# Kernel optimization log

Measured on AMD Instinct MI355X. Metric: run time of the kernel, lower is better.

## Reference

```python
import jax, jax.numpy as jnp
import numpy as np

B, DIM, H, W = 2, 256, 64, 64
HEADS, DIM_HEAD = 8, 64
DIM_INNER = HEADS * DIM_HEAD  # 512


def setup_inputs() -> dict:
    key = jax.random.key(0)
    k1, k2, k3 = jax.random.split(key, 3)
    fmap = jax.random.normal(k1, (B, DIM, H, W), dtype=jnp.float32)
    # 1x1 convs == channel matmuls; store as [out_ch, in_ch]
    w_qkv = jax.random.normal(k2, (3 * DIM_INNER, DIM), dtype=jnp.float32) * (DIM ** -0.5)
    w_out = jax.random.normal(k3, (DIM, DIM_INNER), dtype=jnp.float32) * (DIM_INNER ** -0.5)
    return {"fmap": fmap, "w_qkv": w_qkv, "w_out": w_out}


def reference(fmap, w_qkv, w_out):
    b, c, x, y = fmap.shape
    n = x * y
    h, d = HEADS, DIM_HEAD
    xt = fmap.reshape(b, c, n)                       # [B, C, N]
    qkv = jnp.einsum('oc,bcn->bon', w_qkv, xt)        # [B, 3*h*d, N]
    q, k, v = jnp.split(qkv, 3, axis=1)               # each [B, h*d, N]
    # -> [B, h, N, d]
    to_bhnd = lambda t: t.reshape(b, h, d, n).transpose(0, 1, 3, 2)
    q, k, v = to_bhnd(q), to_bhnd(k), to_bhnd(v)
    # Euclidean distance matrix (torch.cdist p=2)
    q2 = jnp.sum(q * q, axis=-1)                      # [B, h, N]
    k2 = jnp.sum(k * k, axis=-1)                      # [B, h, N]
    qk = jnp.einsum('bhid,bhjd->bhij', q, k)          # [B, h, N, N]
    sim = jnp.sqrt(jnp.maximum(q2[..., :, None] + k2[..., None, :] - 2.0 * qk, 0.0))
    attn = jax.nn.softmax(sim, axis=-1)
    out = jnp.einsum('bhij,bhjd->bhid', attn, v)      # [B, h, N, d]
    out = out.transpose(0, 1, 3, 2).reshape(b, h * d, n)  # [B, h*d, N]
    out = jnp.einsum('oc,bcn->bon', w_out, out)       # [B, dim, N]
    return out.reshape(b, c, x, y)
```

## Files before the change

kernel.cpp:

```cpp
#include <hip/hip_runtime.h>

#define B_      2
#define DIM_    256
#define N_      4096
#define HEADS_  8
#define DINNER_ 512

typedef _Float16 half_t;
typedef _Float16 half8  __attribute__((ext_vector_type(8)));
typedef _Float16 half4v __attribute__((ext_vector_type(4)));
typedef _Float16 half2v __attribute__((ext_vector_type(2)));
typedef float    floatx4 __attribute__((ext_vector_type(4)));

#define SCL_    1.4426950408889634f
#define SHIFT2_ 20.0f


__global__ __launch_bounds__(256) void prep_all(const float* __restrict__ fmap,
                                                const float* __restrict__ w_qkv,
                                                const float* __restrict__ w_out,
                                                half_t* __restrict__ wqF,
                                                half_t* __restrict__ woF,
                                                half_t* __restrict__ xTg) {
    const int t = threadIdx.x, bx = blockIdx.x;
    __shared__ float Tl[64 * 68];
    if (bx < 96) {
        half_t* dst = wqF + (size_t)bx * 4096;
#pragma unroll
        for (int j = 0; j < 2; ++j) {
            const int cch = j * 256 + t;
            const int o = cch >> 4, m15 = cch & 15;
            const float4 a  = *(const float4*)&w_qkv[(size_t)(bx * 16 + m15) * 256 + o * 8];
            const float4 bb = *(const float4*)&w_qkv[(size_t)(bx * 16 + m15) * 256 + o * 8 + 4];
            half8 hv;
            hv[0] = (half_t)a.x;  hv[1] = (half_t)a.y;  hv[2] = (half_t)a.z;  hv[3] = (half_t)a.w;
            hv[4] = (half_t)bb.x; hv[5] = (half_t)bb.y; hv[6] = (half_t)bb.z; hv[7] = (half_t)bb.w;
            *(half8*)(dst + o * 128 + m15 * 8) = hv;
        }
    } else if (bx < 112) {
        const int mt = bx - 96;
        half_t* dst = woF + (size_t)mt * 8192;
#pragma unroll
        for (int j = 0; j < 4; ++j) {
            const int cch = j * 256 + t;
            const int o = cch >> 4, m15 = cch & 15;
            const float4 a  = *(const float4*)&w_out[(size_t)(mt * 16 + m15) * 512 + o * 8];
            const float4 bb = *(const float4*)&w_out[(size_t)(mt * 16 + m15) * 512 + o * 8 + 4];
            half8 hv;
            hv[0] = (half_t)a.x;  hv[1] = (half_t)a.y;  hv[2] = (half_t)a.z;  hv[3] = (half_t)a.w;
            hv[4] = (half_t)bb.x; hv[5] = (half_t)bb.y; hv[6] = (half_t)bb.z; hv[7] = (half_t)bb.w;
            *(half8*)(dst + o * 128 + m15 * 8) = hv;
        }
    } else {
        const int idx = bx - 112;
        const int n0 = (idx & 63) * 64, k0 = ((idx >> 6) & 3) * 64, b = idx >> 8;
        {
            const int kk = t >> 2, nq = (t & 3) * 16;
#pragma unroll
            for (int q = 0; q < 4; ++q) {
                float4 v = *(const float4*)&fmap[((size_t)b * DIM_ + k0 + kk) * N_ + n0 + nq + 4 * q];
                *(float4*)&Tl[kk * 68 + nq + 4 * q] = v;
            }
        }
        __syncthreads();
        {
            const int n = t >> 2, ko = (t & 3) * 16;
            half8 h0, h1;
#pragma unroll
            for (int j = 0; j < 8; ++j) h0[j] = (half_t)Tl[(ko + j) * 68 + n];
#pragma unroll
            for (int j = 0; j < 8; ++j) h1[j] = (half_t)Tl[(ko + 8 + j) * 68 + n];
            half_t* dst = xTg + (((size_t)b * 64 + (n0 >> 6)) * 4 + (k0 >> 6)) * 4096;
            const int o0 = ((ko >> 5) * 4 + (n >> 4)) * 512 + (((ko >> 3) & 3) * 16 + (n & 15)) * 8;
            const int k8 = ko + 8;
            const int o1 = ((k8 >> 5) * 4 + (n >> 4)) * 512 + (((k8 >> 3) & 3) * 16 + (n & 15)) * 8;
            *(half8*)(dst + o0) = h0;
            *(half8*)(dst + o1) = h1;
        }
    }
}

__global__ __launch_bounds__(256) void mm_qkv_mf(const half_t* __restrict__ wqF,
                                                 const half_t* __restrict__ xTg,
                                                 half_t* __restrict__ perm,
                                                 float* __restrict__ sq) {
    const int nt64 = blockIdx.x, by = blockIdx.y, b = blockIdx.z;
    const int t = threadIdx.x, w = t >> 6, L = t & 63, c = L & 15, g = L >> 4;
    const int mt = by * 4 + w;

    const half_t* Ab = wqF + (size_t)mt * 4096;
    const half_t* Bb = xTg + (((size_t)b * 64 + nt64) * 4) * 4096;

    __shared__ __align__(16) char smraw[8192 + 4352];
    half_t* VtH = (half_t*)smraw;
    float*  red = (float*)(smraw + 8192);

    const floatx4 fz = {0.f, 0.f, 0.f, 0.f};
    floatx4 acc[4];
#pragma unroll
    for (int ns = 0; ns < 4; ++ns) acc[ns] = fz;

#pragma unroll
    for (int kc = 0; kc < 8; ++kc) {
        const half8 af = *(const half8*)(Ab + (kc * 4 + g) * 128 + c * 8);
        const half_t* Bs = Bb + (kc >> 1) * 4096 + (kc & 1) * 2048;
#pragma unroll
        for (int ns = 0; ns < 4; ++ns) {
            const half8 bf = *(const half8*)(Bs + ns * 512 + L * 8);
            acc[ns] = __builtin_amdgcn_mfma_f32_16x16x32_f16(af, bf, acc[ns], 0, 0, 0);
        }
    }

    half_t* dst = perm + (((size_t)(b * 24 + by) * 64 + nt64) << 12);
    if (by < 16) {
        float part[4];
#pragma unroll
        for (int ns = 0; ns < 4; ++ns) {
            half_t hv[4];
            float s = 0.f;
#pragma unroll
            for (int i = 0; i < 4; ++i) {
                hv[i] = (half_t)(acc[ns][i] * SCL_);
                const float f = (float)hv[i];
                s = fmaf(f, f, s);
            }
            part[ns] = s;
            const int off = ((w >> 1) * 4 + ns) * 512 + (((2 * w + (g >> 1)) & 3) * 16 + c) * 8 + 4 * (g & 1);
            half2v p0, p1;
            p0[0] = hv[0]; p0[1] = hv[1];
            p1[0] = hv[2]; p1[1] = hv[3];
            *(half2v*)(VtH + off)     = p0;
            *(half2v*)(VtH + off + 2) = p1;
        }
#pragma unroll
        for (int ns = 0; ns < 4; ++ns)
            red[(ns * 16 + (w * 4 + g)) * 17 + c] = part[ns];
        __syncthreads();
#pragma unroll
        for (int j = 0; j < 2; ++j)
            *(half8*)(dst + t * 16 + j * 8) = *(half8*)(VtH + t * 16 + j * 8);
        if (t < 64) {
            const int ns = t >> 4, cc = t & 15;
            float s = 0.f;
#pragma unroll
            for (int wg = 0; wg < 16; ++wg) s += red[(ns * 16 + wg) * 17 + cc];
            const int tens = by >> 3, hh = by & 7;
            sq[((size_t)(tens * 16 + b * 8 + hh)) * N_ + nt64 * 64 + ns * 16 + cc] = s;
        }
    } else {
#pragma unroll
        for (int ns = 0; ns < 4; ++ns)
#pragma unroll
            for (int i = 0; i < 4; ++i)
                VtH[(ns * 4 + w) * 256 + ((c >> 2) * 16 + 4 * g + i) * 4 + (c & 3)] = (half_t)acc[ns][i];
        __syncthreads();
#pragma unroll
        for (int j = 0; j < 2; ++j)
            *(half8*)(dst + t * 16 + j * 8) = *(half8*)(VtH + t * 16 + j * 8);
    }
}

__global__ __launch_bounds__(512) void attn_mfma(const half_t* __restrict__ perm,
                                                 const float* __restrict__ sq,
                                                 half_t* __restrict__ oh,
                                                 float* __restrict__ lbuf) {
    const int bx = blockIdx.x;
    const int qb = bx & 15, kh = bx >> 4;
    const int h = blockIdx.y, b = blockIdx.z;
    const int bh = b * HEADS_ + h;

    const half_t* Qb = perm + ((size_t)(b * 24 + h) << 18);
    const half_t* Kb = perm + ((size_t)(b * 24 + 8 + h) << 18);
    const half_t* Vb = perm + ((size_t)(b * 24 + 16 + h) << 18);
    const float* q2a = sq + (size_t)bh * N_;
    const float* k2a = sq + (size_t)(16 + bh) * N_;

    __shared__ __align__(16) half_t Kl[2][4096];
    __shared__ __align__(16) half_t Vl[2][4096];
    __shared__ __align__(16) float  k2l[1024];

    const int t = threadIdx.x, w = t >> 6, L = t & 63, c = L & 15, g = L >> 4;
    const floatx4 fz = {0.f, 0.f, 0.f, 0.f};

    *(float2*)&k2l[t * 2] = *(const float2*)&k2a[kh * 1024 + t * 2];

    const int tl = w >> 1;
    const int p0 = (w & 1) * 2, p1 = p0 + 1;
    const half_t* Qt = Qb + ((size_t)(qb * 4 + tl) << 12);
    const half8 bq0a = *(const half8*)(Qt + (0 * 4 + p0) * 512 + L * 8);
    const half8 bq1a = *(const half8*)(Qt + (1 * 4 + p0) * 512 + L * 8);
    const half8 bq0b = *(const half8*)(Qt + (0 * 4 + p1) * 512 + L * 8);
    const half8 bq1b = *(const half8*)(Qt + (1 * 4 + p1) * 512 + L * 8);
    const float q2la = q2a[qb * 256 + 64 * tl + 16 * p0 + c];
    const float q2lb = q2a[qb * 256 + 64 * tl + 16 * p1 + c];

    half4v aone;
    {
        const half_t ov = (c == 0) ? (half_t)1.0f : (half_t)0.0f;
        aone[0] = ov; aone[1] = ov; aone[2] = ov; aone[3] = ov;
    }

    floatx4 Oa[4], Ob[4];
    floatx4 laca = fz, lacb = fz;
#pragma unroll
    for (int dt = 0; dt < 4; ++dt) { Oa[dt] = fz; Ob[dt] = fz; }

    const int kt0 = kh * 16;
    half8 rk = *(const half8*)(Kb + ((size_t)kt0 << 12) + t * 8);
    half8 rv = *(const half8*)(Vb + ((size_t)kt0 << 12) + t * 8);

    const int ntrot = w & 3;

    for (int it = 0; it < 16; ++it) {
        const int buf = it & 1;
        *(half8*)(&Kl[buf][t * 8]) = rk;
        *(half8*)(&Vl[buf][t * 8]) = rv;
        asm volatile("s_waitcnt lgkmcnt(0)\n\ts_barrier" ::: "memory");
        if (it < 15) {
            rk = *(const half8*)(Kb + ((size_t)(kt0 + it + 1) << 12) + t * 8);
            rv = *(const half8*)(Vb + ((size_t)(kt0 + it + 1) << 12) + t * 8);
        }

#pragma unroll
        for (int ntx = 0; ntx < 4; ++ntx) {
            const int nt = (ntx + ntrot) & 3;
            const half8 ak0 = *(const half8*)(&Kl[buf][(0 * 4 + nt) * 512 + L * 8]);
            const half8 ak1 = *(const half8*)(&Kl[buf][(1 * 4 + nt) * 512 + L * 8]);
            __builtin_amdgcn_s_setprio(1);
            floatx4 Sa = __builtin_amdgcn_mfma_f32_16x16x32_f16(ak0, bq0a, fz, 0, 0, 0);
            Sa = __builtin_amdgcn_mfma_f32_16x16x32_f16(ak1, bq1a, Sa, 0, 0, 0);
            floatx4 Sb = __builtin_amdgcn_mfma_f32_16x16x32_f16(ak0, bq0b, fz, 0, 0, 0);
            Sb = __builtin_amdgcn_mfma_f32_16x16x32_f16(ak1, bq1b, Sb, 0, 0, 0);
            __builtin_amdgcn_s_setprio(0);
            const float4 k2v = *(const float4*)&k2l[it * 64 + 16 * nt + 4 * g];

            float pa[4], pb[4];
            const float k2arr[4] = {k2v.x, k2v.y, k2v.z, k2v.w};
#pragma unroll
            for (int i = 0; i < 4; ++i) {
                pa[i] = __builtin_amdgcn_exp2f(
                    __builtin_amdgcn_sqrtf(__builtin_fabsf(fmaf(Sa[i], -2.0f, q2la + k2arr[i]))) - SHIFT2_);
                pb[i] = __builtin_amdgcn_exp2f(
                    __builtin_amdgcn_sqrtf(__builtin_fabsf(fmaf(Sb[i], -2.0f, q2lb + k2arr[i]))) - SHIFT2_);
            }
            half4v bpa, bpb;
            {
                const half2v a0 = __builtin_bit_cast(half2v, __builtin_amdgcn_cvt_pkrtz(pa[0], pa[1]));
                const half2v a1 = __builtin_bit_cast(half2v, __builtin_amdgcn_cvt_pkrtz(pa[2], pa[3]));
                bpa[0] = a0[0]; bpa[1] = a0[1]; bpa[2] = a1[0]; bpa[3] = a1[1];
                const half2v b0 = __builtin_bit_cast(half2v, __builtin_amdgcn_cvt_pkrtz(pb[0], pb[1]));
                const half2v b1 = __builtin_bit_cast(half2v, __builtin_amdgcn_cvt_pkrtz(pb[2], pb[3]));
                bpb[0] = b0[0]; bpb[1] = b0[1]; bpb[2] = b1[0]; bpb[3] = b1[1];
            }

            __builtin_amdgcn_s_setprio(1);
            laca = __builtin_amdgcn_mfma_f32_16x16x16f16(aone, bpa, laca, 0, 0, 0);
            lacb = __builtin_amdgcn_mfma_f32_16x16x16f16(aone, bpb, lacb, 0, 0, 0);
#pragma unroll
            for (int dt = 0; dt < 4; ++dt) {
                const half4v av = *(const half4v*)(&Vl[buf][(nt * 4 + dt) * 256 + L * 4]);
                Oa[dt] = __builtin_amdgcn_mfma_f32_16x16x16f16(av, bpa, Oa[dt], 0, 0, 0);
                Ob[dt] = __builtin_amdgcn_mfma_f32_16x16x16f16(av, bpb, Ob[dt], 0, 0, 0);
            }
            __builtin_amdgcn_s_setprio(0);
        }
    }

    const int ntile = qb * 4 + tl;
    half_t* dst = oh + (size_t)kh * 4194304 + (((size_t)bh * 64 + ntile) << 12);
#pragma unroll
    for (int dt = 0; dt < 4; ++dt) {
        const int obase = ((dt >> 1) * 4) * 512 + (((2 * dt + (g >> 1)) & 3) * 16 + c) * 8 + 4 * (g & 1);
        const half2v a0 = __builtin_bit_cast(half2v, __builtin_amdgcn_cvt_pkrtz(Oa[dt][0], Oa[dt][1]));
        const half2v a1 = __builtin_bit_cast(half2v, __builtin_amdgcn_cvt_pkrtz(Oa[dt][2], Oa[dt][3]));
        *(half2v*)(dst + obase + p0 * 512)     = a0;
        *(half2v*)(dst + obase + p0 * 512 + 2) = a1;
        const half2v b0 = __builtin_bit_cast(half2v, __builtin_amdgcn_cvt_pkrtz(Ob[dt][0], Ob[dt][1]));
        const half2v b1 = __builtin_bit_cast(half2v, __builtin_amdgcn_cvt_pkrtz(Ob[dt][2], Ob[dt][3]));
        *(half2v*)(dst + obase + p1 * 512)     = b0;
        *(half2v*)(dst + obase + p1 * 512 + 2) = b1;
    }
    if (L < 16) {
        const size_t lb0 = (size_t)kh * 65536 + (size_t)bh * N_ + qb * 256 + 64 * tl;
        lbuf[lb0 + 16 * p0 + L] = laca[0];
        lbuf[lb0 + 16 * p1 + L] = lacb[0];
    }
}

__global__ __launch_bounds__(256) void mm_out_mf(const half_t* __restrict__ woF,
                                                 const half_t* __restrict__ oh,
                                                 const float* __restrict__ lbuf,
                                                 float* __restrict__ out) {
    const int nt64 = blockIdx.x, mb = blockIdx.y, b = blockIdx.z;
    const int t = threadIdx.x, w = t >> 6, L = t & 63, c = L & 15, g = L >> 4;
    const int mt = mb * 4 + w;

    const half_t* Ab = woF + (size_t)mt * 8192;
    const floatx4 fz = {0.f, 0.f, 0.f, 0.f};
    floatx4 O4[4];
#pragma unroll
    for (int ns = 0; ns < 4; ++ns) O4[ns] = fz;

    __shared__ __align__(16) half_t sh[2][4096];
    __shared__ float lsh[2][64];

    half8 r0[4], r1[4];
    float lr[4];

    auto LOADH = [&](int h) {
        const size_t toff = (((size_t)(b * 8 + h) * 64 + nt64) << 12) + t * 16;
#pragma unroll
        for (int q = 0; q < 4; ++q) {
            r0[q] = *(const half8*)(oh + (size_t)q * 4194304 + toff);
            r1[q] = *(const half8*)(oh + (size_t)q * 4194304 + toff + 8);
        }
        if (t < 64) {
            const size_t li = (size_t)(b * 8 + h) * N_ + nt64 * 64 + t;
#pragma unroll
            for (int q = 0; q < 4; ++q) lr[q] = lbuf[(size_t)q * 65536 + li];
        }
    };

    LOADH(0);
    for (int h = 0; h < 8; ++h) {
        const int buf = h & 1;
        const half8 s0 = (r0[0] + r0[1]) + (r0[2] + r0[3]);
        const half8 s1 = (r1[0] + r1[1]) + (r1[2] + r1[3]);
        *(half8*)(&sh[buf][t * 16])     = s0;
        *(half8*)(&sh[buf][t * 16 + 8]) = s1;
        if (t < 64)
            lsh[buf][t] = __builtin_amdgcn_rcpf((lr[0] + lr[1]) + (lr[2] + lr[3]));
        __syncthreads();
        if (h < 7) LOADH(h + 1);

        floatx4 acc[4];
#pragma unroll
        for (int ns = 0; ns < 4; ++ns) acc[ns] = fz;
#pragma unroll
        for (int c2 = 0; c2 < 2; ++c2) {
            const half8 af = *(const half8*)(Ab + (h * 8 + c2 * 4 + g) * 128 + c * 8);
#pragma unroll
            for (int ns = 0; ns < 4; ++ns) {
                const half8 bf = *(const half8*)(&sh[buf][(c2 * 4 + ns) * 512 + L * 8]);
                acc[ns] = __builtin_amdgcn_mfma_f32_16x16x32_f16(af, bf, acc[ns], 0, 0, 0);
            }
        }
#pragma unroll
        for (int ns = 0; ns < 4; ++ns) {
            const float inv = lsh[buf][ns * 16 + c];
#pragma unroll
            for (int i = 0; i < 4; ++i) O4[ns][i] = fmaf(acc[ns][i], inv, O4[ns][i]);
        }
    }

    float* Cg = out + ((size_t)b * DIM_ + mt * 16) * N_ + nt64 * 64;
#pragma unroll
    for (int ns = 0; ns < 4; ++ns)
#pragma unroll
        for (int i = 0; i < 4; ++i)
            Cg[(size_t)(4 * g + i) * N_ + ns * 16 + c] = O4[ns][i];
}

extern "C" void kernel_launch(void* const* d_in, const int* in_sizes, int n_in,
                              void* d_out, int out_size, void* d_ws, size_t ws_size,
                              hipStream_t stream) {
    const float* fmap  = (const float*)d_in[0];
    const float* w_qkv = (const float*)d_in[1];
    const float* w_out = (const float*)d_in[2];
    float* out = (float*)d_out;

    char* ws = (char*)d_ws;
    half_t* perm = (half_t*)ws;
    float*  sq   = (float*) (ws + 25165824);
    float*  lbuf = (float*) (ws + 25690112);
    half_t* woF  = (half_t*)(ws + 26738688);
    half_t* oh   = (half_t*)(ws + 27000832);
    half_t* xTg  = (half_t*)(ws + 27000832);
    half_t* wqF  = (half_t*)(ws + 31195136);

    prep_all <<<624, 256, 0, stream>>>(fmap, w_qkv, w_out, wqF, woF, xTg);
    mm_qkv_mf<<<dim3(64, 24, 2), 256, 0, stream>>>(wqF, xTg, perm, sq);
    attn_mfma<<<dim3(64, 8, 2), 512, 0, stream>>>(perm, sq, oh, lbuf);
    mm_out_mf<<<dim3(64, 4, 2), 256, 0, stream>>>(woF, oh, lbuf, out);
}
```

Measured before the change: 204.3 us.

## Use K=32 MFMA for PV and row-sum by pairing key tiles, relayout V

```diff
diff --git a/kernel.cpp b/kernel.cpp
--- a/kernel.cpp
+++ b/kernel.cpp
@@ -152,7 +152,8 @@
         for (int ns = 0; ns < 4; ++ns)
 #pragma unroll
             for (int i = 0; i < 4; ++i)
-                VtH[(ns * 4 + w) * 256 + ((c >> 2) * 16 + 4 * g + i) * 4 + (c & 3)] = (half_t)acc[ns][i];
+                VtH[((ns >> 1) * 4 + w) * 512 + ((c >> 2) * 16 + 4 * g + i) * 8 + (ns & 1) * 4 + (c & 3)] =
+                    (half_t)acc[ns][i];
         __syncthreads();
 #pragma unroll
         for (int j = 0; j < 2; ++j)
@@ -194,10 +195,11 @@
     const float q2la = q2a[qb * 256 + 64 * tl + 16 * p0 + c];
     const float q2lb = q2a[qb * 256 + 64 * tl + 16 * p1 + c];
 
-    half4v aone;
+    half8 aone8;
     {
         const half_t ov = (c == 0) ? (half_t)1.0f : (half_t)0.0f;
-        aone[0] = ov; aone[1] = ov; aone[2] = ov; aone[3] = ov;
+        aone8[0] = ov; aone8[1] = ov; aone8[2] = ov; aone8[3] = ov;
+        aone8[4] = ov; aone8[5] = ov; aone8[6] = ov; aone8[7] = ov;
     }
 
     floatx4 Oa[4], Ob[4];
@@ -209,7 +211,7 @@
     half8 rk = *(const half8*)(Kb + ((size_t)kt0 << 12) + t * 8);
     half8 rv = *(const half8*)(Vb + ((size_t)kt0 << 12) + t * 8);
 
-    const int ntrot = w & 3;
+    union H8 { half8 v; half2v h2[4]; };
 
     for (int it = 0; it < 16; ++it) {
         const int buf = it & 1;
@@ -222,47 +224,42 @@
         }
 
 #pragma unroll
-        for (int ntx = 0; ntx < 4; ++ntx) {
-            const int nt = (ntx + ntrot) & 3;
-            const half8 ak0 = *(const half8*)(&Kl[buf][(0 * 4 + nt) * 512 + L * 8]);
-            const half8 ak1 = *(const half8*)(&Kl[buf][(1 * 4 + nt) * 512 + L * 8]);
-            __builtin_amdgcn_s_setprio(1);
-            floatx4 Sa = __builtin_amdgcn_mfma_f32_16x16x32_f16(ak0, bq0a, fz, 0, 0, 0);
-            Sa = __builtin_amdgcn_mfma_f32_16x16x32_f16(ak1, bq1a, Sa, 0, 0, 0);
-            floatx4 Sb = __builtin_amdgcn_mfma_f32_16x16x32_f16(ak0, bq0b, fz, 0, 0, 0);
-            Sb = __builtin_amdgcn_mfma_f32_16x16x32_f16(ak1, bq1b, Sb, 0, 0, 0);
-            __builtin_amdgcn_s_setprio(0);
-            const float4 k2v = *(const float4*)&k2l[it * 64 + 16 * nt + 4 * g];
-
-            float pa[4], pb[4];
-            const float k2arr[4] = {k2v.x, k2v.y, k2v.z, k2v.w};
-#pragma unroll
-            for (int i = 0; i < 4; ++i) {
-                pa[i] = __builtin_amdgcn_exp2f(
-                    __builtin_amdgcn_sqrtf(__builtin_fabsf(fmaf(Sa[i], -2.0f, q2la + k2arr[i]))) - SHIFT2_);
-                pb[i] = __builtin_amdgcn_exp2f(
-                    __builtin_amdgcn_sqrtf(__builtin_fabsf(fmaf(Sb[i], -2.0f, q2lb + k2arr[i]))) - SHIFT2_);
-            }
-            half4v bpa, bpb;
-            {
-                const half2v a0 = __builtin_bit_cast(half2v, __builtin_amdgcn_cvt_pkrtz(pa[0], pa[1]));
-                const half2v a1 = __builtin_bit_cast(half2v, __builtin_amdgcn_cvt_pkrtz(pa[2], pa[3]));
-                bpa[0] = a0[0]; bpa[1] = a0[1]; bpa[2] = a1[0]; bpa[3] = a1[1];
-                const half2v b0 = __builtin_bit_cast(half2v, __builtin_amdgcn_cvt_pkrtz(pb[0], pb[1]));
-                const half2v b1 = __builtin_bit_cast(half2v, __builtin_amdgcn_cvt_pkrtz(pb[2], pb[3]));
-                bpb[0] = b0[0]; bpb[1] = b0[1]; bpb[2] = b1[0]; bpb[3] = b1[1];
-            }
-
-            __builtin_amdgcn_s_setprio(1);
-            laca = __builtin_amdgcn_mfma_f32_16x16x16f16(aone, bpa, laca, 0, 0, 0);
-            lacb = __builtin_amdgcn_mfma_f32_16x16x16f16(aone, bpb, lacb, 0, 0, 0);
+        for (int ntp = 0; ntp < 2; ++ntp) {
+            H8 ua, ub;
+#pragma unroll
+            for (int hh = 0; hh < 2; ++hh) {
+                const int nt = ntp * 2 + hh;
+                const half8 ak0 = *(const half8*)(&Kl[buf][(0 * 4 + nt) * 512 + L * 8]);
+                const half8 ak1 = *(const half8*)(&Kl[buf][(1 * 4 + nt) * 512 + L * 8]);
+                floatx4 Sa = __builtin_amdgcn_mfma_f32_16x16x32_f16(ak0, bq0a, fz, 0, 0, 0);
+                Sa = __builtin_amdgcn_mfma_f32_16x16x32_f16(ak1, bq1a, Sa, 0, 0, 0);
+                floatx4 Sb = __builtin_amdgcn_mfma_f32_16x16x32_f16(ak0, bq0b, fz, 0, 0, 0);
+                Sb = __builtin_amdgcn_mfma_f32_16x16x32_f16(ak1, bq1b, Sb, 0, 0, 0);
+                const float4 k2v = *(const float4*)&k2l[it * 64 + 16 * nt + 4 * g];
+
+                float pa[4], pb[4];
+                const float k2arr[4] = {k2v.x, k2v.y, k2v.z, k2v.w};
+#pragma unroll
+                for (int i = 0; i < 4; ++i) {
+                    pa[i] = __builtin_amdgcn_exp2f(
+                        __builtin_amdgcn_sqrtf(__builtin_fabsf(fmaf(Sa[i], -2.0f, q2la + k2arr[i]))) - SHIFT2_);
+                    pb[i] = __builtin_amdgcn_exp2f(
+                        __builtin_amdgcn_sqrtf(__builtin_fabsf(fmaf(Sb[i], -2.0f, q2lb + k2arr[i]))) - SHIFT2_);
+                }
+                ua.h2[2 * hh]     = __builtin_bit_cast(half2v, __builtin_amdgcn_cvt_pkrtz(pa[0], pa[1]));
+                ua.h2[2 * hh + 1] = __builtin_bit_cast(half2v, __builtin_amdgcn_cvt_pkrtz(pa[2], pa[3]));
+                ub.h2[2 * hh]     = __builtin_bit_cast(half2v, __builtin_amdgcn_cvt_pkrtz(pb[0], pb[1]));
+                ub.h2[2 * hh + 1] = __builtin_bit_cast(half2v, __builtin_amdgcn_cvt_pkrtz(pb[2], pb[3]));
+            }
+
+            laca = __builtin_amdgcn_mfma_f32_16x16x32_f16(aone8, ua.v, laca, 0, 0, 0);
+            lacb = __builtin_amdgcn_mfma_f32_16x16x32_f16(aone8, ub.v, lacb, 0, 0, 0);
 #pragma unroll
             for (int dt = 0; dt < 4; ++dt) {
-                const half4v av = *(const half4v*)(&Vl[buf][(nt * 4 + dt) * 256 + L * 4]);
-                Oa[dt] = __builtin_amdgcn_mfma_f32_16x16x16f16(av, bpa, Oa[dt], 0, 0, 0);
-                Ob[dt] = __builtin_amdgcn_mfma_f32_16x16x16f16(av, bpb, Ob[dt], 0, 0, 0);
-            }
-            __builtin_amdgcn_s_setprio(0);
+                const half8 av = *(const half8*)(&Vl[buf][(ntp * 4 + dt) * 512 + L * 8]);
+                Oa[dt] = __builtin_amdgcn_mfma_f32_16x16x32_f16(av, ua.v, Oa[dt], 0, 0, 0);
+                Ob[dt] = __builtin_amdgcn_mfma_f32_16x16x32_f16(av, ub.v, Ob[dt], 0, 0, 0);
+            }
         }
     }
 
```

Result: faster. 191.0 us (-6.5%).
